# Optimization experiments

Measured on AMD Instinct MI355X. Metric: run time of the kernel, lower is better.

## Reference

```python
import jax, jax.numpy as jnp
import numpy as np

B, C, L = 32, 128, 4096
TIME_DIM = 512
K_TOP = 8


def setup_inputs() -> dict:
    key = jax.random.key(0)
    k1, k2, k3, k4 = jax.random.split(key, 4)
    x = jax.random.normal(k1, (B, C, L), dtype=jnp.float32)
    time_emb = jax.random.normal(k2, (B, TIME_DIM), dtype=jnp.float32)
    # nn.Linear(time_dim, channels): weight (C, time_dim), bias (C,)
    W = jax.random.normal(k3, (C, TIME_DIM), dtype=jnp.float32) / np.sqrt(TIME_DIM)
    b = jax.random.normal(k4, (C,), dtype=jnp.float32) * 0.01
    return {"x": x, "time_emb": time_emb, "W": W, "b": b}


def reference(x, time_emb, W, b):
    Bn, Cn, n = x.shape
    k = min(K_TOP, n // 2 + 1)
    # time-conditioned modulation: Linear -> tanh -> (1 + tanh) scale
    scale = time_emb @ W.T + b                      # (B, C)
    x_mod = x * (1.0 + jnp.tanh(scale))[:, :, None]  # (B, C, L)
    # rFFT along time
    x_fft = jnp.fft.rfft(x_mod, axis=-1)             # (B, C, F) complex64
    amp = jnp.abs(x_fft)
    # top-k frequency bins per (b, c) row
    _, topk_idx = jax.lax.top_k(amp, k)              # (B, C, k)
    gathered = jnp.take_along_axis(x_fft, topk_idx, axis=-1)
    bi = jnp.arange(Bn)[:, None, None]
    ci = jnp.arange(Cn)[None, :, None]
    masked_fft = jnp.zeros_like(x_fft).at[bi, ci, topk_idx].set(gathered)
    p_it = jnp.fft.irfft(masked_fft, n=n, axis=-1)
    return p_it.astype(x.dtype)
```

## Files before the change

kernel.cpp:

```cpp
#include <hip/hip_runtime.h>

#define LL 4096
#define THREADS 512
#define KK 8

typedef float v2f __attribute__((ext_vector_type(2)));

#define PD(i) ((i) + ((i) >> 3))
#define PERM8(r) ((((r) & 3) << 1) | ((r) >> 2))

__device__ __forceinline__ float sinr(float x) {
    float r; asm("v_sin_f32 %0, %1" : "=v"(r) : "v"(x)); return r;
}
__device__ __forceinline__ float cosr(float x) {
    float r; asm("v_cos_f32 %0, %1" : "=v"(r) : "v"(x)); return r;
}

__device__ __forceinline__ v2f cmulw(v2f z, v2f w) {
    v2f zs = __builtin_shufflevector(z, z, 1, 0);
    v2f res = z * (v2f){w.x, w.x};
    res += zs * (v2f){w.y, -w.y};
    return res;
}
__device__ __forceinline__ v2f cmul(v2f a, v2f b) {
    v2f as = __builtin_shufflevector(a, a, 1, 0);
    v2f res = a * (v2f){b.x, b.x};
    res += as * (v2f){-b.y, b.y};
    return res;
}

__device__ __forceinline__ void dft4(v2f& a, v2f& b, v2f& c, v2f& d) {
    v2f t0 = a + c, t1 = a - c, t2 = b + d, t3 = b - d;
    a = t0 + t2; c = t0 - t2;
    v2f t3n = (v2f){t3.y, -t3.x};
    b = t1 + t3n; d = t1 - t3n;
}

__device__ __forceinline__ void dft8(v2f* v) {
    dft4(v[0], v[2], v[4], v[6]);
    dft4(v[1], v[3], v[5], v[7]);
    const float C2 = 0.70710678118654752f;
    v[3] = cmulw(v[3], (v2f){C2, C2});
    v[5] = (v2f){v[5].y, -v[5].x};
    v[7] = cmulw(v[7], (v2f){-C2, C2});
#pragma unroll
    for (int k0 = 0; k0 < 4; ++k0) {
        v2f a = v[2 * k0], b = v[2 * k0 + 1];
        v[2 * k0]     = a + b;
        v[2 * k0 + 1] = a - b;
    }
}

__device__ __forceinline__ void twiddle7(v2f* v, float th) {
    v2f w1 = (v2f){cosr(th), sinr(th)};
    v2f w = w1;
    v[1] = cmulw(v[1], w);
#pragma unroll
    for (int r = 2; r < 8; ++r) {
        w = cmul(w, w1);
        v[r] = cmulw(v[r], w);
    }
}

__global__ __launch_bounds__(THREADS, 8)
void fft2_topk_k(const float* __restrict__ x, const float* __restrict__ te,
                 const float* __restrict__ W, const float* __restrict__ bias,
                 float* __restrict__ out) {
    __shared__ v2f zb[4608];
    __shared__ float wv[8];
    __shared__ float candV[2][16];
    __shared__ int   candB[2][16];
    __shared__ v2f  selAB[2][KK];
    __shared__ v2f  selST[2][KK];
    __shared__ int  selF[2][KK];

    int t = threadIdx.x;
    int pair = blockIdx.x;
    int b = pair >> 6;
    int c0 = (pair & 63) << 1;
    int row0 = (b << 7) + c0;

    {
        int mh = t >> 8, tt = t & 255;
        const float* tp = te + b * 512;
        const float* wp = W + (c0 + mh) * 512;
        float ps = tp[tt] * wp[tt] + tp[tt + 256] * wp[tt + 256];
#pragma unroll
        for (int off = 32; off; off >>= 1) ps += __shfl_down(ps, off);
        if ((t & 63) == 0) wv[t >> 6] = ps;
    }

    const float* xp0 = x + (size_t)row0 * LL;
    const float* xp1 = xp0 + LL;
    v2f v[8];
#pragma unroll
    for (int r = 0; r < 8; ++r) { v[r].x = xp0[t + 512 * r]; v[r].y = xp1[t + 512 * r]; }
    __syncthreads();
    float g0 = 1.0f + tanhf(wv[0] + wv[1] + wv[2] + wv[3] + bias[c0]);
    float g1 = 1.0f + tanhf(wv[4] + wv[5] + wv[6] + wv[7] + bias[c0 + 1]);
    {
        v2f g = (v2f){g0, g1};
#pragma unroll
        for (int r = 0; r < 8; ++r) v[r] *= g;
    }

    dft8(v);
    {
        int wb = 9 * t;
#pragma unroll
        for (int r = 0; r < 8; ++r) zb[wb + r] = v[PERM8(r)];
    }
    __syncthreads();

    int rb = t + (t >> 3);

#pragma unroll
    for (int r = 0; r < 8; ++r) v[r] = zb[rb + 576 * r];
    twiddle7(v, (float)(t & 7) * (1.0f / 64.0f));
    dft8(v);
    __syncthreads();
    {
        int wb = 72 * (t >> 3) + (t & 7);
#pragma unroll
        for (int r = 0; r < 8; ++r) zb[wb + 9 * r] = v[PERM8(r)];
    }
    __syncthreads();

#pragma unroll
    for (int r = 0; r < 8; ++r) v[r] = zb[rb + 576 * r];
    twiddle7(v, (float)(t & 63) * (1.0f / 512.0f));
    dft8(v);
    __syncthreads();
    {
        int l6 = t & 63;
        int wb = 576 * (t >> 6) + l6 + (l6 >> 3);
#pragma unroll
        for (int r = 0; r < 8; ++r) zb[wb + 72 * r] = v[PERM8(r)];
    }
    __syncthreads();

#pragma unroll
    for (int r = 0; r < 8; ++r) v[r] = zb[rb + 576 * r];
    twiddle7(v, (float)t * (1.0f / 4096.0f));
    dft8(v);
#pragma unroll
    for (int r = 0; r < 8; ++r) zb[rb + 576 * r] = v[PERM8(r)];
    __syncthreads();

    int wid = t >> 6, lane = t & 63;

    if (wid < 4) {
        int row = wid >> 1, hf = wid & 1;
        int kb = (hf << 10) + lane;
        float amp[16];
        float lv = -1.f; int lm = 0;
#pragma unroll
        for (int m = 0; m < 16; ++m) {
            int k = kb + (m << 6);
            v2f z = zb[PD(k)];
            v2f y = zb[PD((4096 - k) & 4095)];
            float Xr = row ? (z.y + y.y) : (z.x + y.x);
            float Xi = row ? (y.x - z.x) : (z.y - y.y);
            float a = Xr * Xr + Xi * Xi;
            amp[m] = a;
            if (a > lv) { lv = a; lm = m; }
        }
        for (int it = 0; it < KK; ++it) {
            float bv = lv; int bb = kb + (lm << 6);
#pragma unroll
            for (int off = 32; off; off >>= 1) {
                float ov = __shfl_down(bv, off);
                int   ob = __shfl_down(bb, off);
                if (ov > bv || (ov == bv && ob < bb)) { bv = ov; bb = ob; }
            }
            if (lane == 0) { candV[row][(hf << 3) + it] = bv; candB[row][(hf << 3) + it] = bb; }
            int wbin = __shfl(bb, 0);
            int rel = wbin - (hf << 10);
            if ((rel & 63) == lane) {
                int m0 = rel >> 6;
                lv = -1.f; lm = 0;
#pragma unroll
                for (int m = 0; m < 16; ++m) {
                    float a = (m == m0) ? -1.f : amp[m];
                    amp[m] = a;
                    if (a > lv) { lv = a; lm = m; }
                }
            }
        }
    }
    __syncthreads();

    if (wid < 2 && lane < 17) {
        int row = wid;
        v2f z2 = zb[PD(2048)];
        float xn = 2.f * (row ? z2.y : z2.x);
        float a2048 = xn * xn;
        float myv; int myb, rank;
        if (lane < 16) {
            myv = candV[row][lane]; myb = candB[row][lane];
            rank = lane & 7;
            int ob = (lane < 8) ? 8 : 0;
#pragma unroll
            for (int j = 0; j < 8; ++j) {
                float ov = candV[row][ob + j]; int obn = candB[row][ob + j];
                if (ov > myv || (ov == myv && obn < myb)) rank++;
            }
            if (a2048 > myv) rank++;
        } else {
            myv = a2048; myb = 2048; rank = 0;
#pragma unroll
            for (int j = 0; j < 16; ++j)
                if (candV[row][j] >= myv) rank++;
        }
        if (rank < KK) {
            v2f z = zb[PD(myb)];
            v2f y = zb[PD((4096 - myb) & 4095)];
            v2f X;
            if (row == 0) X = (v2f){0.5f * (z.x + y.x), 0.5f * (z.y - y.y)};
            else          X = (v2f){0.5f * (z.y + y.y), 0.5f * (y.x - z.x)};
            bool edge = (myb == 0) || (myb == 2048);
            float wgt = edge ? 1.f : 2.f;
            selF[row][rank] = myb;
            selAB[row][rank] = (v2f){wgt * (1.0f / 4096.0f) * X.x,
                                     edge ? 0.f : wgt * (1.0f / 4096.0f) * X.y};
            float a = (float)((myb & 15) << 8) * (1.0f / 4096.0f);
            selST[row][rank] = (v2f){cosr(a), sinr(a)};
        }
    }
    __syncthreads();

    {
        int mh = t >> 8, u = t & 255;
        v2f w[KK], st[KK]; float sg[KK];
        const float i4096 = 1.0f / 4096.0f;
#pragma unroll
        for (int k = 0; k < KK; ++k) {
            int f = selF[mh][k];
            int m0 = (f * u) & 4095;
            float a0 = (float)m0 * i4096;
            w[k] = cmul(selAB[mh][k], (v2f){cosr(a0), sinr(a0)});
            st[k] = selST[mh][k];
            sg[k] = (f & 1) ? -1.f : 1.f;
        }
        float* op = out + (size_t)(row0 + mh) * LL;
#pragma unroll 1
        for (int q = 0; q < 8; ++q) {
            float acc = 0.f, acd = 0.f;
#pragma unroll
            for (int k = 0; k < KK; ++k) {
                acc += w[k].x;
                acd = fmaf(sg[k], w[k].x, acd);
                w[k] = cmul(w[k], st[k]);
            }
            op[u + (q << 8)] = acc;
            op[u + (q << 8) + 2048] = acd;
        }
    }
}

extern "C" void kernel_launch(void* const* d_in, const int* in_sizes, int n_in,
                              void* d_out, int out_size, void* d_ws, size_t ws_size,
                              hipStream_t stream) {
    const float* x    = (const float*)d_in[0];
    const float* te   = (const float*)d_in[1];
    const float* W    = (const float*)d_in[2];
    const float* bias = (const float*)d_in[3];
    float* out = (float*)d_out;
    fft2_topk_k<<<2048, THREADS, 0, stream>>>(x, te, W, bias, out);
}
```

Before: 55.37 us.

## Shrink LDS padding, use power-tree twiddles, Chebyshev recurrence in top-k synthesis

Padding in the shared FFT buffer changes from one slot per 8 to one per 16, shrinking LDS use, and the transpose store addresses are reworked to match. Twiddle powers are now built as a shallow product tree instead of a serial chain, which shortens the dependency chain. The inverse synthesis of the top-k bins replaces the per-step complex multiply with a real Chebyshev recurrence (2cos·x − prev), packed two bins per vector and fully unrolled. The recurrence can accumulate slightly different rounding error, and the new padding may bring back some LDS bank conflicts.

```diff
diff --git a/kernel.cpp b/kernel.cpp
--- a/kernel.cpp
+++ b/kernel.cpp
@@ -6,7 +6,7 @@
 
 typedef float v2f __attribute__((ext_vector_type(2)));
 
-#define PD(i) ((i) + ((i) >> 3))
+#define PD(i) ((i) + ((i) >> 4))
 #define PERM8(r) ((((r) & 3) << 1) | ((r) >> 2))
 
 __device__ __forceinline__ float sinr(float x) {
@@ -53,25 +53,30 @@
 
 __device__ __forceinline__ void twiddle7(v2f* v, float th) {
     v2f w1 = (v2f){cosr(th), sinr(th)};
-    v2f w = w1;
-    v[1] = cmulw(v[1], w);
-#pragma unroll
-    for (int r = 2; r < 8; ++r) {
-        w = cmul(w, w1);
-        v[r] = cmulw(v[r], w);
-    }
+    v2f w2 = cmul(w1, w1);
+    v2f w3 = cmul(w2, w1);
+    v2f w4 = cmul(w2, w2);
+    v2f w5 = cmul(w3, w2);
+    v2f w6 = cmul(w3, w3);
+    v2f w7 = cmul(w4, w3);
+    v[1] = cmulw(v[1], w1);
+    v[2] = cmulw(v[2], w2);
+    v[3] = cmulw(v[3], w3);
+    v[4] = cmulw(v[4], w4);
+    v[5] = cmulw(v[5], w5);
+    v[6] = cmulw(v[6], w6);
+    v[7] = cmulw(v[7], w7);
 }
 
 __global__ __launch_bounds__(THREADS, 8)
 void fft2_topk_k(const float* __restrict__ x, const float* __restrict__ te,
                  const float* __restrict__ W, const float* __restrict__ bias,
                  float* __restrict__ out) {
-    __shared__ v2f zb[4608];
+    __shared__ v2f zb[4352];
     __shared__ float wv[8];
     __shared__ float candV[2][16];
     __shared__ int   candB[2][16];
     __shared__ v2f  selAB[2][KK];
-    __shared__ v2f  selST[2][KK];
     __shared__ int  selF[2][KK];
 
     int t = threadIdx.x;
@@ -106,45 +111,50 @@
 
     dft8(v);
     {
-        int wb = 9 * t;
+        int wb = 8 * t + (t >> 1);
 #pragma unroll
         for (int r = 0; r < 8; ++r) zb[wb + r] = v[PERM8(r)];
     }
     __syncthreads();
 
-    int rb = t + (t >> 3);
-
-#pragma unroll
-    for (int r = 0; r < 8; ++r) v[r] = zb[rb + 576 * r];
+    int rb = t + (t >> 4);
+
+#pragma unroll
+    for (int r = 0; r < 8; ++r) v[r] = zb[rb + 544 * r];
     twiddle7(v, (float)(t & 7) * (1.0f / 64.0f));
     dft8(v);
     __syncthreads();
     {
-        int wb = 72 * (t >> 3) + (t & 7);
-#pragma unroll
-        for (int r = 0; r < 8; ++r) zb[wb + 9 * r] = v[PERM8(r)];
-    }
-    __syncthreads();
-
-#pragma unroll
-    for (int r = 0; r < 8; ++r) v[r] = zb[rb + 576 * r];
+        int wb = 64 * (t >> 3) + (t & 7);
+        int B0 = wb + (wb >> 4);
+        int B1 = (wb + 8) + ((wb + 8) >> 4);
+#pragma unroll
+        for (int s = 0; s < 4; ++s) {
+            zb[B0 + 17 * s] = v[PERM8(2 * s)];
+            zb[B1 + 17 * s] = v[PERM8(2 * s + 1)];
+        }
+    }
+    __syncthreads();
+
+#pragma unroll
+    for (int r = 0; r < 8; ++r) v[r] = zb[rb + 544 * r];
     twiddle7(v, (float)(t & 63) * (1.0f / 512.0f));
     dft8(v);
     __syncthreads();
     {
-        int l6 = t & 63;
-        int wb = 576 * (t >> 6) + l6 + (l6 >> 3);
-#pragma unroll
-        for (int r = 0; r < 8; ++r) zb[wb + 72 * r] = v[PERM8(r)];
-    }
-    __syncthreads();
-
-#pragma unroll
-    for (int r = 0; r < 8; ++r) v[r] = zb[rb + 576 * r];
+        int wb = 512 * (t >> 6) + (t & 63);
+        int B2 = wb + (wb >> 4);
+#pragma unroll
+        for (int r = 0; r < 8; ++r) zb[B2 + 68 * r] = v[PERM8(r)];
+    }
+    __syncthreads();
+
+#pragma unroll
+    for (int r = 0; r < 8; ++r) v[r] = zb[rb + 544 * r];
     twiddle7(v, (float)t * (1.0f / 4096.0f));
     dft8(v);
 #pragma unroll
-    for (int r = 0; r < 8; ++r) zb[rb + 576 * r] = v[PERM8(r)];
+    for (int r = 0; r < 8; ++r) zb[rb + 544 * r] = v[PERM8(r)];
     __syncthreads();
 
     int wid = t >> 6, lane = t & 63;
@@ -158,7 +168,8 @@
         for (int m = 0; m < 16; ++m) {
             int k = kb + (m << 6);
             v2f z = zb[PD(k)];
-            v2f y = zb[PD((4096 - k) & 4095)];
+            int kq = (4096 - k) & 4095;
+            v2f y = zb[PD(kq)];
             float Xr = row ? (z.y + y.y) : (z.x + y.x);
             float Xi = row ? (y.x - z.x) : (z.y - y.y);
             float a = Xr * Xr + Xi * Xi;
@@ -214,7 +225,8 @@
         }
         if (rank < KK) {
             v2f z = zb[PD(myb)];
-            v2f y = zb[PD((4096 - myb) & 4095)];
+            int mq = (4096 - myb) & 4095;
+            v2f y = zb[PD(mq)];
             v2f X;
             if (row == 0) X = (v2f){0.5f * (z.x + y.x), 0.5f * (z.y - y.y)};
             else          X = (v2f){0.5f * (z.y + y.y), 0.5f * (y.x - z.x)};
@@ -223,37 +235,48 @@
             selF[row][rank] = myb;
             selAB[row][rank] = (v2f){wgt * (1.0f / 4096.0f) * X.x,
                                      edge ? 0.f : wgt * (1.0f / 4096.0f) * X.y};
-            float a = (float)((myb & 15) << 8) * (1.0f / 4096.0f);
-            selST[row][rank] = (v2f){cosr(a), sinr(a)};
         }
     }
     __syncthreads();
 
     {
         int mh = t >> 8, u = t & 255;
-        v2f w[KK], st[KK]; float sg[KK];
         const float i4096 = 1.0f / 4096.0f;
-#pragma unroll
-        for (int k = 0; k < KK; ++k) {
-            int f = selF[mh][k];
-            int m0 = (f * u) & 4095;
-            float a0 = (float)m0 * i4096;
-            w[k] = cmul(selAB[mh][k], (v2f){cosr(a0), sinr(a0)});
-            st[k] = selST[mh][k];
-            sg[k] = (f & 1) ? -1.f : 1.f;
+        v2f rc[4], rp[4], tcv[4], sgv[4];
+#pragma unroll
+        for (int j = 0; j < 4; ++j) {
+            int f0 = selF[mh][2 * j], f1 = selF[mh][2 * j + 1];
+            v2f A0 = selAB[mh][2 * j], A1 = selAB[mh][2 * j + 1];
+            int m0a = (f0 * u) & 4095, m0b = (f1 * u) & 4095;
+            float c0a = cosr((float)m0a * i4096), s0a = sinr((float)m0a * i4096);
+            float c0b = cosr((float)m0b * i4096), s0b = sinr((float)m0b * i4096);
+            float r0a = A0.x * c0a - A0.y * s0a;
+            float i0a = A0.x * s0a + A0.y * c0a;
+            float r0b = A1.x * c0b - A1.y * s0b;
+            float i0b = A1.x * s0b + A1.y * c0b;
+            float da = (float)((f0 & 15) << 8) * i4096;
+            float db = (float)((f1 & 15) << 8) * i4096;
+            float cda = cosr(da), sda = sinr(da);
+            float cdb = cosr(db), sdb = sinr(db);
+            rc[j] = (v2f){r0a, r0b};
+            rp[j] = (v2f){r0a * cda + i0a * sda, r0b * cdb + i0b * sdb};
+            tcv[j] = (v2f){cda + cda, cdb + cdb};
+            sgv[j] = (v2f){(f0 & 1) ? -1.f : 1.f, (f1 & 1) ? -1.f : 1.f};
         }
         float* op = out + (size_t)(row0 + mh) * LL;
-#pragma unroll 1
+#pragma unroll
         for (int q = 0; q < 8; ++q) {
-            float acc = 0.f, acd = 0.f;
-#pragma unroll
-            for (int k = 0; k < KK; ++k) {
-                acc += w[k].x;
-                acd = fmaf(sg[k], w[k].x, acd);
-                w[k] = cmul(w[k], st[k]);
-            }
-            op[u + (q << 8)] = acc;
-            op[u + (q << 8) + 2048] = acd;
+            v2f accv = (rc[0] + rc[1]) + (rc[2] + rc[3]);
+            v2f acdv = rc[0] * sgv[0] + rc[1] * sgv[1]
+                     + rc[2] * sgv[2] + rc[3] * sgv[3];
+            op[u + (q << 8)] = accv.x + accv.y;
+            op[u + (q << 8) + 2048] = acdv.x + acdv.y;
+#pragma unroll
+            for (int j = 0; j < 4; ++j) {
+                v2f rn = tcv[j] * rc[j] - rp[j];
+                rp[j] = rc[j];
+                rc[j] = rn;
+            }
         }
     }
 }
```

New measurement: 53.07 us. 4.1% less time.
